# Optimization experiments

Hardware: AMD Instinct MI355X
Metric: run time of the kernel (lower is better)

The kernel has to match this reference:

```python
import jax, jax.numpy as jnp
import numpy as np

B, S, E, H = 2, 2048, 1024, 8
DH = E // H


def setup_inputs() -> dict:
    key = jax.random.key(0)
    ks = jax.random.split(key, 8)
    sc = 1.0 / np.sqrt(E)
    return {
        "q": jax.random.normal(ks[0], (B, S, E), jnp.float32),
        "k": jax.random.normal(ks[1], (B, S, E), jnp.float32),
        "v": jax.random.normal(ks[2], (B, S, E), jnp.float32),
        "Wq": jax.random.normal(ks[3], (E, E), jnp.float32) * sc,
        "bq": jnp.zeros((E,), jnp.float32),
        "Wk": jax.random.normal(ks[4], (E, E), jnp.float32) * sc,
        "bk": jnp.zeros((E,), jnp.float32),
        "Wv": jax.random.normal(ks[5], (E, E), jnp.float32) * sc,
        "bv": jnp.zeros((E,), jnp.float32),
        "Wo": jax.random.normal(ks[6], (E, E), jnp.float32) * sc,
        "bo": jnp.zeros((E,), jnp.float32),
        "is_causal": 1,
    }


def reference(q, k, v, Wq, bq, Wk, bk, Wv, bv, Wo, bo, is_causal):
    # q,k,v: [B,S,E]. Dense projections, split into H heads of dim DH.
    def heads(x, W, b):
        y = x @ W + b                       # [B,S,E]
        return y.reshape(B, S, H, DH).transpose(0, 2, 1, 3)  # [B,H,S,DH]

    qh = heads(q, Wq, bq)
    kh = heads(k, Wk, bk)
    vh = heads(v, Wv, bv)

    scale = 1.0 / jnp.sqrt(jnp.asarray(DH, q.dtype))
    scores = jnp.einsum("bhsd,bhtd->bhst", qh, kh) * scale  # [B,H,S,S]

    if is_causal:
        # tril mask (BigBird layout is all-ones here; causality comes from attn_mask)
        causal = jnp.tril(jnp.ones((S, S), bool))
        neg = jnp.asarray(jnp.finfo(scores.dtype).min, scores.dtype)
        scores = jnp.where(causal[None, None], scores, neg)

    attn = jax.nn.softmax(scores, axis=-1)                  # [B,H,S,S]
    ctx = jnp.einsum("bhst,bhtd->bhsd", attn, vh)           # [B,H,S,DH]
    ctx = ctx.transpose(0, 2, 1, 3).reshape(B, S, E)        # merge heads
    return ctx @ Wo + bo
```

## Files before the change

kernel.cpp:

```cpp
#include <hip/hip_runtime.h>
#include <math.h>


typedef __bf16 bf16_t;
typedef __bf16 bf16x8 __attribute__((ext_vector_type(8)));
typedef float f32x4 __attribute__((ext_vector_type(4)));

#define MFMA16(a, b, c) __builtin_amdgcn_mfma_f32_16x16x32_bf16(a, b, c, 0, 0, 0)

__global__ __launch_bounds__(256) void prep(const float* q, const float* k,
                                            const float* v, bf16_t* qb,
                                            bf16_t* kb, bf16_t* vb,
                                            const float* W0, const float* W1,
                                            const float* W2, const float* W3,
                                            bf16_t* Wt) {
  const int bid = blockIdx.x, tid = threadIdx.x;
  if (bid < 6144) {
    const int z = bid >> 11, chunk = bid & 2047;
    const float* x = (z == 0) ? q : (z == 1) ? k : v;
    bf16_t* y = (z == 0) ? qb : (z == 1) ? kb : vb;
    size_t i = ((size_t)chunk * 256 + tid) * 8;
    float4 a = *(const float4*)(x + i);
    float4 b = *(const float4*)(x + i + 4);
    bf16x8 o = {(bf16_t)a.x, (bf16_t)a.y, (bf16_t)a.z, (bf16_t)a.w,
                (bf16_t)b.x, (bf16_t)b.y, (bf16_t)b.z, (bf16_t)b.w};
    *(bf16x8*)(y + i) = o;
  } else {
    __shared__ float t[32][33];
    const int b2 = bid - 6144;
    const int wz = b2 >> 10, t2 = b2 & 1023;
    const float* W = (wz == 0) ? W0 : (wz == 1) ? W1 : (wz == 2) ? W2 : W3;
    bf16_t* o = Wt + (size_t)wz * 1024 * 1024;
    const int n0 = (t2 & 31) * 32, k0 = (t2 >> 5) * 32;
    const int tx = tid & 31, ty = tid >> 5;
#pragma unroll
    for (int i = 0; i < 4; i++)
      t[ty + 8 * i][tx] = W[(size_t)(k0 + ty + 8 * i) * 1024 + n0 + tx];
    __syncthreads();
#pragma unroll
    for (int i = 0; i < 4; i++)
      o[(size_t)(n0 + ty + 8 * i) * 1024 + k0 + tx] = (bf16_t)t[tx][ty + 8 * i];
  }
}

template <int MODE>
__global__ __launch_bounds__(256) void gemm_k(
    const bf16_t* qb, const bf16_t* kb, const bf16_t* vb, const bf16_t* Wt,
    const float* b0, const float* b1, const float* b2, bf16_t* Qh, bf16_t* Kh,
    bf16_t* Vt, float* Of32) {
  __shared__ bf16_t As[2][128 * 64];
  __shared__ bf16_t Bs[2][128 * 64];
  const int tid = threadIdx.x, w = tid >> 6, lane = tid & 63;
  const int bm = blockIdx.x, bn = blockIdx.y;
  const int wr = w >> 1, wc = w & 1, q4 = lane >> 4, lo = lane & 15;
  const int z = (MODE == 0) ? blockIdx.z : 3;
  const bf16_t* A = (MODE == 1) ? qb : (z == 0) ? qb : (z == 1) ? kb : vb;
  const bf16_t* Bt = Wt + (size_t)z * 1024 * 1024;
  const float* bias = (MODE == 1) ? b0 : (z == 0) ? b0 : (z == 1) ? b1 : b2;

  f32x4 acc[4][4];
#pragma unroll
  for (int m = 0; m < 4; m++)
#pragma unroll
    for (int n = 0; n < 4; n++) acc[m][n] = (f32x4){0.f, 0.f, 0.f, 0.f};

  const int r2 = tid >> 1;
  const int cb = (tid & 1) * 4;
  const bf16_t* Arow = A + (size_t)(bm * 128 + r2) * 1024;
  const bf16_t* Brow = Bt + (size_t)(bn * 128 + r2) * 1024;

  bf16x8 ar[4], br[4];
  auto loadAB = [&](int k0) {
#pragma unroll
    for (int i = 0; i < 4; i++) {
      ar[i] = *(const bf16x8*)(Arow + k0 + (cb + i) * 8);
      br[i] = *(const bf16x8*)(Brow + k0 + (cb + i) * 8);
    }
  };

  loadAB(0);
  for (int k = 0; k < 16; k++) {
    const int cur = k & 1;
#pragma unroll
    for (int i = 0; i < 4; i++) {
      *(bf16x8*)&As[cur][r2 * 64 + (((cb + i) ^ (r2 & 7)) * 8)] = ar[i];
      *(bf16x8*)&Bs[cur][r2 * 64 + (((cb + i) ^ (r2 & 7)) * 8)] = br[i];
    }
    if (k < 15) loadAB((k + 1) * 64);
    __syncthreads();

#pragma unroll
    for (int kc = 0; kc < 2; kc++) {
      bf16x8 af[4], bfr[4];
#pragma unroll
      for (int m = 0; m < 4; m++) {
        int rr = wr * 64 + m * 16 + lo;
        af[m] = *(const bf16x8*)&As[cur][rr * 64 + (((kc * 4 + q4) ^ (rr & 7)) * 8)];
      }
#pragma unroll
      for (int n = 0; n < 4; n++) {
        int rr = wc * 64 + n * 16 + lo;
        bfr[n] = *(const bf16x8*)&Bs[cur][rr * 64 + (((kc * 4 + q4) ^ (rr & 7)) * 8)];
      }
#pragma unroll
      for (int m = 0; m < 4; m++)
#pragma unroll
        for (int n = 0; n < 4; n++)
          acc[m][n] = MFMA16(af[m], bfr[n], acc[m][n]);
    }
  }

#pragma unroll
  for (int m = 0; m < 4; m++) {
#pragma unroll
    for (int n = 0; n < 4; n++) {
      int rowg0 = bm * 128 + wr * 64 + m * 16 + q4 * 4;
      int colg = bn * 128 + wc * 64 + n * 16 + lo;
      float bv = bias[colg];
#pragma unroll
      for (int rg = 0; rg < 4; rg++) {
        float val = acc[m][n][rg] + bv;
        int row = rowg0 + rg;
        if (MODE == 1) {
          Of32[(size_t)row * 1024 + colg] = val;
        } else {
          int b = row >> 11, s = row & 2047;
          int h = colg >> 7, d = colg & 127;
          if (z == 0)
            Qh[(((size_t)(b * 8 + h)) * 2048 + s) * 128 + d] = (bf16_t)val;
          else if (z == 1)
            Kh[(((size_t)(b * 8 + h)) * 2048 + s) * 128 + d] = (bf16_t)val;
          else
            Vt[(((size_t)(b * 8 + h)) * 128 + d) * 2048 + s] = (bf16_t)val;
        }
      }
    }
  }
}

__global__ __launch_bounds__(256) void flash_k(const bf16_t* Qh,
                                               const bf16_t* Kh,
                                               const bf16_t* Vt, bf16_t* ctx,
                                               const int* causal_p) {
  __shared__ bf16_t sm[32768 + 4 * 32 * 88];
  const int tid = threadIdx.x, w = tid >> 6, lane = tid & 63;
  const int q4 = lane >> 4, lo = lane & 15;
  const int n0 = blockIdx.x;
  const int bh = n0 & 15, t = n0 >> 4;
  const int causal = *causal_p;
  const int kmax = causal ? 2 * t + 1 : 31;

  bf16_t* Ps = sm + 32768 + w * (32 * 88);

  bf16x8 aq[2][4];
#pragma unroll
  for (int s = 0; s < 2; s++) {
    const bf16_t* qa =
        Qh + ((size_t)bh * 2048 + t * 128 + w * 32 + s * 16 + lo) * 128;
#pragma unroll
    for (int ks = 0; ks < 4; ks++)
      aq[s][ks] = *(const bf16x8*)(qa + ks * 32 + q4 * 8);
  }

  const bf16_t* Kbase = Kh + (size_t)bh * 2048 * 128;
  const bf16_t* Vbase = Vt + (size_t)bh * 128 * 2048;
  const int kr = tid >> 2, kc = (tid & 3) * 4;
  const int vd = tid >> 1, vc = (tid & 1) * 4;

  bf16x8 kreg[4], vreg[4];
  auto loadKV = [&](int kt) {
    const bf16_t* kp = Kbase + (size_t)(kt * 64 + kr) * 128;
    const bf16_t* vp = Vbase + (size_t)vd * 2048 + kt * 64;
#pragma unroll
    for (int i = 0; i < 4; i++) {
      kreg[i] = *(const bf16x8*)(kp + (kc + i) * 8);
      vreg[i] = *(const bf16x8*)(vp + (vc + i) * 8);
    }
  };

  f32x4 acc[2][8];
  f32x4 lacc[2];
#pragma unroll
  for (int s = 0; s < 2; s++) {
#pragma unroll
    for (int i = 0; i < 8; i++) acc[s][i] = (f32x4){0.f, 0.f, 0.f, 0.f};
    lacc[s] = (f32x4){0.f, 0.f, 0.f, 0.f};
  }

  const bf16_t one = (bf16_t)1.0f;
  const bf16x8 vone = {one, one, one, one, one, one, one, one};
  const float sc2 = 0.08838834764831845f * 1.44269504088896f;

  loadKV(0);
  for (int kt = 0; kt <= kmax; ++kt) {
    bf16_t* Kd = sm + (kt & 1) * 8192;
    bf16_t* Vd = sm + 16384 + (kt & 1) * 8192;
#pragma unroll
    for (int i = 0; i < 4; i++)
      *(bf16x8*)&Kd[kr * 128 + (((kc + i) ^ (kr & 7)) * 8)] = kreg[i];
#pragma unroll
    for (int i = 0; i < 4; i++)
      *(bf16x8*)&Vd[vd * 64 + (((vc + i) ^ ((vd >> 1) & 7)) * 8)] = vreg[i];
    if (kt < kmax) loadKV(kt + 1);
    __syncthreads();

    f32x4 sa[2][4];
#pragma unroll
    for (int s = 0; s < 2; s++)
#pragma unroll
      for (int nt = 0; nt < 4; nt++) sa[s][nt] = (f32x4){0.f, 0.f, 0.f, 0.f};
#pragma unroll
    for (int ks = 0; ks < 4; ks++) {
#pragma unroll
      for (int nt = 0; nt < 4; nt++) {
        int key = nt * 16 + lo;
        bf16x8 bk =
            *(const bf16x8*)&Kd[key * 128 + (((ks * 4 + q4) ^ (key & 7)) * 8)];
        sa[0][nt] = MFMA16(aq[0][ks], bk, sa[0][nt]);
        sa[1][nt] = MFMA16(aq[1][ks], bk, sa[1][nt]);
      }
    }

    const bool diag = causal && (kt >= 2 * t);
    const int keyg0 = kt * 64;
    const int rowg0 = t * 128 + w * 32 + q4 * 4;
#pragma unroll
    for (int s = 0; s < 2; s++) {
#pragma unroll
      for (int nt = 0; nt < 4; nt++) {
        int keyg = keyg0 + nt * 16 + lo;
#pragma unroll
        for (int rg = 0; rg < 4; rg++) {
          float pv = exp2f(sa[s][nt][rg] * sc2);
          if (diag && keyg > rowg0 + s * 16 + rg) pv = 0.f;
          Ps[(s * 16 + q4 * 4 + rg) * 88 + nt * 16 + lo] = (bf16_t)pv;
        }
      }
    }

    bf16x8 ap0[2], ap1[2];
#pragma unroll
    for (int s = 0; s < 2; s++) {
      ap0[s] = *(const bf16x8*)&Ps[(s * 16 + lo) * 88 + q4 * 8];
      ap1[s] = *(const bf16x8*)&Ps[(s * 16 + lo) * 88 + 32 + q4 * 8];
      lacc[s] = MFMA16(ap0[s], vone, lacc[s]);
      lacc[s] = MFMA16(ap1[s], vone, lacc[s]);
    }
#pragma unroll
    for (int n = 0; n < 8; n++) {
      int d = n * 16 + lo;
      int sw = (d >> 1) & 7;
      bf16x8 bv0 = *(const bf16x8*)&Vd[d * 64 + ((q4 ^ sw) * 8)];
      bf16x8 bv1 = *(const bf16x8*)&Vd[d * 64 + (((4 + q4) ^ sw) * 8)];
#pragma unroll
      for (int s = 0; s < 2; s++) {
        acc[s][n] = MFMA16(ap0[s], bv0, acc[s][n]);
        acc[s][n] = MFMA16(ap1[s], bv1, acc[s][n]);
      }
    }
  }

  int b = bh >> 3, h = bh & 7;
#pragma unroll
  for (int s = 0; s < 2; s++) {
#pragma unroll
    for (int rg = 0; rg < 4; rg++) {
      float inv = 1.f / lacc[s][rg];
      int r = b * 2048 + t * 128 + w * 32 + s * 16 + q4 * 4 + rg;
#pragma unroll
      for (int n = 0; n < 8; n++)
        ctx[(size_t)r * 1024 + h * 128 + n * 16 + lo] =
            (bf16_t)(acc[s][n][rg] * inv);
    }
  }
}

extern "C" void kernel_launch(void* const* d_in, const int* in_sizes, int n_in,
                              void* d_out, int out_size, void* d_ws,
                              size_t ws_size, hipStream_t stream) {
  const float* q = (const float*)d_in[0];
  const float* k = (const float*)d_in[1];
  const float* v = (const float*)d_in[2];
  const float* Wq = (const float*)d_in[3];
  const float* bq = (const float*)d_in[4];
  const float* Wk = (const float*)d_in[5];
  const float* bk = (const float*)d_in[6];
  const float* Wv = (const float*)d_in[7];
  const float* bv = (const float*)d_in[8];
  const float* Wo = (const float*)d_in[9];
  const float* bo = (const float*)d_in[10];
  const int* isc = (const int*)d_in[11];

  char* ws = (char*)d_ws;
  bf16_t* Wt = (bf16_t*)ws;
  bf16_t* qb = (bf16_t*)(ws + (8ull << 20));
  bf16_t* kb = (bf16_t*)(ws + (16ull << 20));
  bf16_t* vb = (bf16_t*)(ws + (24ull << 20));
  bf16_t* Qh = (bf16_t*)(ws + (32ull << 20));
  bf16_t* Kh = (bf16_t*)(ws + (40ull << 20));
  bf16_t* Vt = (bf16_t*)(ws + (48ull << 20));
  bf16_t* ctx = (bf16_t*)(ws + (8ull << 20));

  prep<<<dim3(10240), 256, 0, stream>>>(q, k, v, qb, kb, vb, Wq, Wk, Wv, Wo, Wt);

  gemm_k<0><<<dim3(32, 8, 3), 256, 0, stream>>>(qb, kb, vb, Wt, bq, bk, bv, Qh,
                                                Kh, Vt, nullptr);

  flash_k<<<dim3(256), 256, 0, stream>>>(Qh, Kh, Vt, ctx, isc);

  gemm_k<1><<<dim3(32, 8), 256, 0, stream>>>(ctx, nullptr, nullptr, Wt, bo,
                                             nullptr, nullptr, nullptr, nullptr,
                                             nullptr, (float*)d_out);
}
```

Before: 250.7 us.

## Halve flash query tile, split keys across warps, reorder blocks for causal balance

The flash kernel now uses 64-query tiles per block, doubling the grid to 512 blocks. The four warps form two row groups, and each group splits every 64-key tile into two 32-key halves. Partial accumulators and row sums are reduced through shared memory at the end. Block indices are mapped so the second half of the grid processes tiles in reverse order, which pairs long and short causal rows to balance load. This raises occupancy and parallelism on the 256-CU device, at the cost of a shared-memory reduction and more redundant K/V loads per query row.

Measured after the change: 228.2 us. 9.0% less time.

```diff
diff --git a/kernel.cpp b/kernel.cpp
--- a/kernel.cpp
+++ b/kernel.cpp
@@ -142,24 +142,27 @@
                                                const bf16_t* Kh,
                                                const bf16_t* Vt, bf16_t* ctx,
                                                const int* causal_p) {
-  __shared__ bf16_t sm[32768 + 4 * 32 * 88];
+  __shared__ bf16_t sm[32768 + 4 * 1280];
   const int tid = threadIdx.x, w = tid >> 6, lane = tid & 63;
   const int q4 = lane >> 4, lo = lane & 15;
+  const int r = w >> 1, kh = w & 1;
   const int n0 = blockIdx.x;
-  const int bh = n0 & 15, t = n0 >> 4;
+  const int u = n0 & 255, hi = n0 >> 8;
+  const int bh = u & 15, p0 = u >> 4;
+  const int t = hi ? (31 - p0) : p0;
   const int causal = *causal_p;
-  const int kmax = causal ? 2 * t + 1 : 31;
-
-  bf16_t* Ps = sm + 32768 + w * (32 * 88);
+  const int kmax = causal ? t : 31;
+
+  bf16_t* Ps = sm + 32768 + w * 1280;
 
   bf16x8 aq[2][4];
 #pragma unroll
-  for (int s = 0; s < 2; s++) {
+  for (int m = 0; m < 2; m++) {
     const bf16_t* qa =
-        Qh + ((size_t)bh * 2048 + t * 128 + w * 32 + s * 16 + lo) * 128;
+        Qh + ((size_t)bh * 2048 + t * 64 + r * 32 + m * 16 + lo) * 128;
 #pragma unroll
     for (int ks = 0; ks < 4; ks++)
-      aq[s][ks] = *(const bf16x8*)(qa + ks * 32 + q4 * 8);
+      aq[m][ks] = *(const bf16x8*)(qa + ks * 32 + q4 * 8);
   }
 
   const bf16_t* Kbase = Kh + (size_t)bh * 2048 * 128;
@@ -181,10 +184,10 @@
   f32x4 acc[2][8];
   f32x4 lacc[2];
 #pragma unroll
-  for (int s = 0; s < 2; s++) {
-#pragma unroll
-    for (int i = 0; i < 8; i++) acc[s][i] = (f32x4){0.f, 0.f, 0.f, 0.f};
-    lacc[s] = (f32x4){0.f, 0.f, 0.f, 0.f};
+  for (int m = 0; m < 2; m++) {
+#pragma unroll
+    for (int i = 0; i < 8; i++) acc[m][i] = (f32x4){0.f, 0.f, 0.f, 0.f};
+    lacc[m] = (f32x4){0.f, 0.f, 0.f, 0.f};
   }
 
   const bf16_t one = (bf16_t)1.0f;
@@ -204,16 +207,16 @@
     if (kt < kmax) loadKV(kt + 1);
     __syncthreads();
 
-    f32x4 sa[2][4];
-#pragma unroll
-    for (int s = 0; s < 2; s++)
-#pragma unroll
-      for (int nt = 0; nt < 4; nt++) sa[s][nt] = (f32x4){0.f, 0.f, 0.f, 0.f};
+    f32x4 sa[2][2];
+#pragma unroll
+    for (int m = 0; m < 2; m++)
+#pragma unroll
+      for (int nt = 0; nt < 2; nt++) sa[m][nt] = (f32x4){0.f, 0.f, 0.f, 0.f};
 #pragma unroll
     for (int ks = 0; ks < 4; ks++) {
 #pragma unroll
-      for (int nt = 0; nt < 4; nt++) {
-        int key = nt * 16 + lo;
+      for (int nt = 0; nt < 2; nt++) {
+        int key = kh * 32 + nt * 16 + lo;
         bf16x8 bk =
             *(const bf16x8*)&Kd[key * 128 + (((ks * 4 + q4) ^ (key & 7)) * 8)];
         sa[0][nt] = MFMA16(aq[0][ks], bk, sa[0][nt]);
@@ -221,56 +224,78 @@
       }
     }
 
-    const bool diag = causal && (kt >= 2 * t);
-    const int keyg0 = kt * 64;
-    const int rowg0 = t * 128 + w * 32 + q4 * 4;
-#pragma unroll
-    for (int s = 0; s < 2; s++) {
-#pragma unroll
-      for (int nt = 0; nt < 4; nt++) {
-        int keyg = keyg0 + nt * 16 + lo;
+    const bool diag = causal && (kt == t);
+#pragma unroll
+    for (int m = 0; m < 2; m++) {
+#pragma unroll
+      for (int nt = 0; nt < 2; nt++) {
+        int keyrel = kh * 32 + nt * 16 + lo;
 #pragma unroll
         for (int rg = 0; rg < 4; rg++) {
-          float pv = exp2f(sa[s][nt][rg] * sc2);
-          if (diag && keyg > rowg0 + s * 16 + rg) pv = 0.f;
-          Ps[(s * 16 + q4 * 4 + rg) * 88 + nt * 16 + lo] = (bf16_t)pv;
+          int rowrel = r * 32 + m * 16 + q4 * 4 + rg;
+          float pv = exp2f(sa[m][nt][rg] * sc2);
+          if (diag && keyrel > rowrel) pv = 0.f;
+          Ps[(m * 16 + q4 * 4 + rg) * 40 + nt * 16 + lo] = (bf16_t)pv;
         }
       }
     }
 
-    bf16x8 ap0[2], ap1[2];
-#pragma unroll
-    for (int s = 0; s < 2; s++) {
-      ap0[s] = *(const bf16x8*)&Ps[(s * 16 + lo) * 88 + q4 * 8];
-      ap1[s] = *(const bf16x8*)&Ps[(s * 16 + lo) * 88 + 32 + q4 * 8];
-      lacc[s] = MFMA16(ap0[s], vone, lacc[s]);
-      lacc[s] = MFMA16(ap1[s], vone, lacc[s]);
+    bf16x8 ap[2];
+#pragma unroll
+    for (int m = 0; m < 2; m++) {
+      ap[m] = *(const bf16x8*)&Ps[(m * 16 + lo) * 40 + q4 * 8];
+      lacc[m] = MFMA16(ap[m], vone, lacc[m]);
     }
 #pragma unroll
     for (int n = 0; n < 8; n++) {
       int d = n * 16 + lo;
       int sw = (d >> 1) & 7;
-      bf16x8 bv0 = *(const bf16x8*)&Vd[d * 64 + ((q4 ^ sw) * 8)];
-      bf16x8 bv1 = *(const bf16x8*)&Vd[d * 64 + (((4 + q4) ^ sw) * 8)];
-#pragma unroll
-      for (int s = 0; s < 2; s++) {
-        acc[s][n] = MFMA16(ap0[s], bv0, acc[s][n]);
-        acc[s][n] = MFMA16(ap1[s], bv1, acc[s][n]);
-      }
-    }
-  }
-
-  int b = bh >> 3, h = bh & 7;
-#pragma unroll
-  for (int s = 0; s < 2; s++) {
-#pragma unroll
-    for (int rg = 0; rg < 4; rg++) {
-      float inv = 1.f / lacc[s][rg];
-      int r = b * 2048 + t * 128 + w * 32 + s * 16 + q4 * 4 + rg;
-#pragma unroll
-      for (int n = 0; n < 8; n++)
-        ctx[(size_t)r * 1024 + h * 128 + n * 16 + lo] =
-            (bf16_t)(acc[s][n][rg] * inv);
+      bf16x8 bv = *(const bf16x8*)&Vd[d * 64 + (((kh * 4 + q4) ^ sw) * 8)];
+      acc[0][n] = MFMA16(ap[0], bv, acc[0][n]);
+      acc[1][n] = MFMA16(ap[1], bv, acc[1][n]);
+    }
+  }
+
+  __syncthreads();
+  float* farena = (float*)sm;
+  if (kh == 1) {
+    int base = r * 4096 + lane * 64;
+#pragma unroll
+    for (int m = 0; m < 2; m++)
+#pragma unroll
+      for (int n = 0; n < 8; n++) {
+        int c = m * 8 + n;
+        *(f32x4*)&farena[base + ((c ^ (lane & 15)) & 15) * 4] = acc[m][n];
+      }
+    float* lp = (float*)(sm + 32768 + w * 1280);
+    *(f32x4*)&lp[lane * 8] = lacc[0];
+    *(f32x4*)&lp[lane * 8 + 4] = lacc[1];
+  }
+  __syncthreads();
+  if (kh == 0) {
+    int base = r * 4096 + lane * 64;
+    float* lp = (float*)(sm + 32768 + (w + 1) * 1280);
+    lacc[0] += *(const f32x4*)&lp[lane * 8];
+    lacc[1] += *(const f32x4*)&lp[lane * 8 + 4];
+#pragma unroll
+    for (int m = 0; m < 2; m++)
+#pragma unroll
+      for (int n = 0; n < 8; n++) {
+        int c = m * 8 + n;
+        acc[m][n] += *(const f32x4*)&farena[base + ((c ^ (lane & 15)) & 15) * 4];
+      }
+    int b = bh >> 3, h = bh & 7;
+#pragma unroll
+    for (int m = 0; m < 2; m++) {
+#pragma unroll
+      for (int rg = 0; rg < 4; rg++) {
+        float inv = 1.f / lacc[m][rg];
+        int row = b * 2048 + t * 64 + r * 32 + m * 16 + q4 * 4 + rg;
+#pragma unroll
+        for (int n = 0; n < 8; n++)
+          ctx[(size_t)row * 1024 + h * 128 + n * 16 + lo] =
+              (bf16_t)(acc[m][n][rg] * inv);
+      }
     }
   }
 }
@@ -306,7 +331,7 @@
   gemm_k<0><<<dim3(32, 8, 3), 256, 0, stream>>>(qb, kb, vb, Wt, bq, bk, bv, Qh,
                                                 Kh, Vt, nullptr);
 
-  flash_k<<<dim3(256), 256, 0, stream>>>(Qh, Kh, Vt, ctx, isc);
+  flash_k<<<dim3(512), 256, 0, stream>>>(Qh, Kh, Vt, ctx, isc);
 
   gemm_k<1><<<dim3(32, 8), 256, 0, stream>>>(ctx, nullptr, nullptr, Wt, bo,
                                              nullptr, nullptr, nullptr, nullptr,
```
